# Optimization experiments

Hardware: AMD Instinct MI355X
Metric: run time of the kernel (lower is better)

The kernel has to match this reference:

```python
import jax, jax.numpy as jnp
import numpy as np

KSIZE = 13
PAD = KSIZE // 2
EPS = 1e-5
MIN_DISP = 1e-3  # clamp to avoid inf depth at zero disparity


def _unfold(x):
    # B,C,H,W -> B, C*k*k, H, W  (im2col with 'same' padding, stride 1; matches F.unfold)
    return jax.lax.conv_general_dilated_patches(
        x, filter_shape=(KSIZE, KSIZE), window_strides=(1, 1),
        padding=[(PAD, PAD), (PAD, PAD)])


def _znorm(p):
    # zero-mean, unit-norm over patch dim -> ZNCC becomes a plain dot product
    p = p - p.mean(axis=1, keepdims=True)
    return p / (jnp.linalg.norm(p, axis=1, keepdims=True) + EPS)


def setup_inputs() -> dict:
    key = jax.random.key(0)
    k1, k2 = jax.random.split(key)
    B, C, H, W = 1, 3, 192, 320
    l_image = jax.random.uniform(k1, (B, C, H, W), jnp.float32)
    # right image = horizontally shifted left + small noise so true matches exist
    r_image = jnp.roll(l_image, shift=-8, axis=-1) + 0.01 * jax.random.normal(k2, (B, C, H, W), jnp.float32)
    fx = 240.0
    intri = jnp.array([[[fx, 0.0, W / 2.0], [0.0, fx, H / 2.0], [0.0, 0.0, 1.0]]], jnp.float32)
    l_extri = jnp.eye(4, dtype=jnp.float32)[None]
    r_extri = l_extri.at[:, 0, 3].set(0.54)  # 0.54 m stereo baseline
    return {"l_image": l_image, "r_image": r_image, "l_intri": intri,
            "r_intri": intri, "l_extri": l_extri, "r_extri": r_extri}


def reference(l_image, r_image, l_intri, r_intri, l_extri, r_extri):
    B, C, H, W = l_image.shape
    # patch unfold (im2col) + ZNCC normalization
    ln = _znorm(_unfold(l_image).reshape(1, -1, H, W))  # 1,D,H,W
    rn = _znorm(_unfold(r_image).reshape(1, -1, H, W))
    # full-width correlation volume: each left pixel vs every right column in its row
    vol = jnp.einsum('bdhw,bdhv->bhwv', ln, rn)  # 1,H,W,W
    # reduce=True -> best-matching right column index
    corresp = jnp.argmax(vol, axis=-1).astype(l_image.dtype)  # 1,H,W
    disp = jnp.abs(corresp - jnp.arange(W, dtype=l_image.dtype))
    # disparity -> depth: depth = fx * baseline / disp
    fx = l_intri[:, 0, 0]
    rel = r_extri @ jnp.linalg.inv(l_extri)  # relative right<-left transform
    baseline = jnp.linalg.norm(rel[:, :3, 3], axis=-1)
    depth = fx[:, None, None] * baseline[:, None, None] / jnp.clip(disp, MIN_DISP, None)
    return depth
```

## Files before the change

### kernel.cpp

```cpp
#include <hip/hip_runtime.h>
#include <math.h>

#define HH 192
#define WW 320
#define DTOT 507.0f
#define KD 39
#define NSPAN 5
#define NCHUNK 5
#define XS 64
#define TV 64
#define TX 76
#define TU 80
#define TUW 76
#define TIS 76
#define TD2 77
#define NPIX (HH*WW)

__global__ void prep_kernel(const float* __restrict__ li, const float* __restrict__ le,
                            const float* __restrict__ re, float* __restrict__ sc,
                            unsigned long long* __restrict__ keys) {
    int t = blockIdx.x * blockDim.x + threadIdx.x;
    if (keys != nullptr && t < NPIX) keys[t] = 0ull;
    if (t == 0) {
        float a[4][4], inv[4][4];
        for (int i = 0; i < 4; ++i)
            for (int j = 0; j < 4; ++j) { a[i][j] = le[i*4+j]; inv[i][j] = (i == j) ? 1.0f : 0.0f; }
        for (int c = 0; c < 4; ++c) {
            int p = c; float mx = fabsf(a[c][c]);
            for (int r = c+1; r < 4; ++r) { float v = fabsf(a[r][c]); if (v > mx) { mx = v; p = r; } }
            if (p != c) for (int j = 0; j < 4; ++j) {
                float tq = a[c][j]; a[c][j] = a[p][j]; a[p][j] = tq;
                tq = inv[c][j]; inv[c][j] = inv[p][j]; inv[p][j] = tq;
            }
            float id = 1.0f / a[c][c];
            for (int j = 0; j < 4; ++j) { a[c][j] *= id; inv[c][j] *= id; }
            for (int r = 0; r < 4; ++r) if (r != c) {
                float f = a[r][c];
                for (int j = 0; j < 4; ++j) { a[r][j] -= f*a[c][j]; inv[r][j] -= f*inv[c][j]; }
            }
        }
        float rel[3];
        for (int i = 0; i < 3; ++i)
            rel[i] = re[i*4+0]*inv[0][3] + re[i*4+1]*inv[1][3] + re[i*4+2]*inv[2][3] + re[i*4+3]*inv[3][3];
        float baseline = sqrtf(rel[0]*rel[0] + rel[1]*rel[1] + rel[2]*rel[2]);
        sc[0] = li[0] * baseline;
    }
}

__global__ __launch_bounds__(256) void match_kernel(
        const float* __restrict__ limg, const float* __restrict__ rimg,
        unsigned long long* __restrict__ sink, int mode) {
    __shared__ float Ls[KD][TX];
    __shared__ float Rs[KD][TU];
    __shared__ float Tc[TU][TIS];
    __shared__ float colL[TX];
    __shared__ float colR1[TUW];
    __shared__ float colR2[TUW];
    __shared__ float smuR[TV];
    __shared__ float sivR[TV];
    __shared__ float redS[4][XS];
    __shared__ int   redV[4][XS];

    const int span = blockIdx.x;
    const int h    = blockIdx.y;
    const int ch   = blockIdx.z;
    const int wlo  = span * XS;
    const int ulo  = ch * TV;
    const int tid  = threadIdx.x;
    const int lane = tid & 63;
    const int wave = tid >> 6;

    for (int i2 = tid; i2 < KD*38; i2 += 256) {
        int k = i2 / 38, q = i2 - k*38;
        int c = k / 13, dy = k - c*13;
        int y = h - 6 + dy, x0 = wlo - 6 + 2*q;
        float2 v = make_float2(0.0f, 0.0f);
        if ((unsigned)y < (unsigned)HH) {
            const float* row = &limg[(c*HH + y)*WW];
            if ((unsigned)x0 < (unsigned)(WW-1)) {
                v = *(const float2*)&row[x0];
            } else {
                if ((unsigned)x0 < (unsigned)WW) v.x = row[x0];
                if ((unsigned)(x0+1) < (unsigned)WW) v.y = row[x0+1];
            }
        }
        *(float2*)&Ls[k][2*q] = v;
    }
    for (int i2 = tid; i2 < KD*40; i2 += 256) {
        int k = i2 / 40, q = i2 - k*40;
        int c = k / 13, dy = k - c*13;
        int y = h - 6 + dy, u0 = ulo - 6 + 2*q;
        float2 v = make_float2(0.0f, 0.0f);
        if ((unsigned)y < (unsigned)HH) {
            const float* row = &rimg[(c*HH + y)*WW];
            if ((unsigned)u0 < (unsigned)(WW-1)) {
                v = *(const float2*)&row[u0];
            } else {
                if ((unsigned)u0 < (unsigned)WW) v.x = row[u0];
                if ((unsigned)(u0+1) < (unsigned)WW) v.y = row[u0+1];
            }
        }
        *(float2*)&Rs[k][2*q] = v;
    }
    __syncthreads();

    if (tid < TX) {
        float s = 0.0f;
        for (int k = 0; k < KD; ++k) s += Ls[k][tid];
        colL[tid] = s;
    } else if (tid >= 128 && tid < 128 + TUW) {
        int c = tid - 128;
        float s1 = 0.0f, s2 = 0.0f;
        for (int k = 0; k < KD; ++k) {
            float v = Rs[k][c];
            s1 += v;
            s2 = fmaf(v, v, s2);
        }
        colR1[c] = s1;
        colR2[c] = s2;
    }
    __syncthreads();

    float muL;
    {
        float s = 0.0f;
        #pragma unroll
        for (int dx = 0; dx < 13; ++dx) s += colL[lane + dx];
        muL = s / DTOT;
    }

    if (tid < 190) {
        const int ti = tid % 19, tj = tid / 19;
        const int i0 = ti * 4, j0 = tj * 8;
        float a[4][8];
        #pragma unroll
        for (int r = 0; r < 4; ++r)
            #pragma unroll
            for (int c = 0; c < 8; ++c) a[r][c] = 0.0f;
        __builtin_amdgcn_s_setprio(1);
        for (int k = 0; k < KD; ++k) {
            float4 la = *(const float4*)&Ls[k][i0];
            float4 r0 = *(const float4*)&Rs[k][j0];
            float4 r1 = *(const float4*)&Rs[k][j0+4];
            float lx[4] = {la.x, la.y, la.z, la.w};
            float rx[8] = {r0.x, r0.y, r0.z, r0.w, r1.x, r1.y, r1.z, r1.w};
            #pragma unroll
            for (int r = 0; r < 4; ++r)
                #pragma unroll
                for (int c = 0; c < 8; ++c)
                    a[r][c] = fmaf(lx[r], rx[c], a[r][c]);
        }
        __builtin_amdgcn_s_setprio(0);
        #pragma unroll
        for (int c = 0; c < 8; ++c)
            *(float4*)&Tc[j0+c][i0] = make_float4(a[0][c], a[1][c], a[2][c], a[3][c]);
    } else if (tid >= 192) {
        int vcc = tid - 192;
        float s1 = 0.0f, s2 = 0.0f;
        #pragma unroll
        for (int dx = 0; dx < 13; ++dx) { s1 += colR1[vcc + dx]; s2 += colR2[vcc + dx]; }
        float mu = s1 / DTOT;
        float var = fmaxf(s2 - s1*s1/DTOT, 0.0f);
        smuR[vcc] = mu;
        sivR[vcc] = 1.0f / (sqrtf(var) + 1e-5f);
    }
    __syncthreads();

    float best = -1e30f;
    int bestv = 0;
    const float dml = DTOT * muL;
    for (int vi = 0; vi < 16; ++vi) {
        int vc = wave * 16 + vi;
        const float* tp0 = &Tc[vc][0] + lane;
        float S = 0.0f;
        int boff = 0;
        #pragma unroll
        for (int g = 0; g < 3; ++g) {
            asm volatile("" : "+v"(boff));
            float y0 = tp0[boff];
            float y1 = tp0[boff + TD2];
            float y2 = tp0[boff + 2*TD2];
            float y3 = tp0[boff + 3*TD2];
            S += y0; S += y1; S += y2; S += y3;
            boff += 4*TD2;
        }
        S += tp0[12*TD2];
        float score = (S - dml * smuR[vc]) * sivR[vc];
        int v = ulo + vc;
        if (score > best) { best = score; bestv = v; }
    }

    redS[wave][lane] = best;
    redV[wave][lane] = bestv;
    __syncthreads();
    if (tid < XS) {
        float b = redS[0][tid]; int bv = redV[0][tid];
        for (int wv = 1; wv < 4; ++wv) {
            float s = redS[wv][tid]; int v2 = redV[wv][tid];
            if (s > b || (s == b && v2 < bv)) { b = s; bv = v2; }
        }
        unsigned ob = __float_as_uint(b);
        ob = (ob & 0x80000000u) ? ~ob : (ob | 0x80000000u);
        unsigned long long key = ((unsigned long long)ob << 32) | (unsigned)(~(unsigned)bv);
        if (mode) {
            sink[(size_t)ch * NPIX + h*WW + wlo + tid] = key;
        } else {
            atomicMax(&sink[h*WW + wlo + tid], key);
        }
    }
}

__global__ __launch_bounds__(256) void depth_kernel(const unsigned long long* __restrict__ sink,
                                                    const float* __restrict__ sc,
                                                    float* __restrict__ out, int mode) {
    int t = blockIdx.x * 256 + threadIdx.x;
    unsigned long long k = sink[t];
    if (mode) {
        #pragma unroll
        for (int p = 1; p < NCHUNK; ++p) {
            unsigned long long k2 = sink[(size_t)p * NPIX + t];
            if (k2 > k) k = k2;
        }
    }
    int v = (int)(~(unsigned int)k);
    float w = (float)(t % WW);
    float disp = fmaxf(fabsf((float)v - w), 0.001f);
    out[t] = sc[0] / disp;
}

__global__ __launch_bounds__(256) void match_fallback(
        const float* __restrict__ limg, const float* __restrict__ rimg,
        const float* __restrict__ ws, float* __restrict__ out) {
    __shared__ float Ls[KD][76];
    __shared__ float Rs[KD][76];
    __shared__ float Tt[76][81];
    __shared__ float colL[76];
    __shared__ float colR1[76];
    __shared__ float colR2[76];
    __shared__ float smuR[64];
    __shared__ float sivR[64];
    __shared__ float redS[4][64];
    __shared__ int   redV[4][64];

    const int span = blockIdx.x;
    const int h    = blockIdx.y;
    const int wlo  = span * 64;
    const int tid  = threadIdx.x;
    const int lane = tid & 63;
    const int wave = tid >> 6;

    for (int i = tid; i < KD*76; i += 256) {
        int k = i / 76, xl = i % 76;
        int c = k / 13, dy = k % 13;
        int y = h - 6 + dy, x = wlo - 6 + xl;
        float v = 0.0f;
        if (y >= 0 && y < HH && x >= 0 && x < WW) v = limg[(c*HH + y)*WW + x];
        Ls[k][xl] = v;
    }
    __syncthreads();

    if (tid < 76) {
        float s = 0.0f;
        for (int k = 0; k < KD; ++k) s += Ls[k][tid];
        colL[tid] = s;
    }
    __syncthreads();

    float muL;
    {
        float s = 0.0f;
        #pragma unroll
        for (int dx = 0; dx < 13; ++dx) s += colL[lane + dx];
        muL = s / DTOT;
    }

    float best = -1e30f;
    int bestv = 0;

    for (int ch = 0; ch < NCHUNK; ++ch) {
        const int ulo = ch * 64;
        for (int i = tid; i < KD*76; i += 256) {
            int k = i / 76, uc = i % 76;
            int c = k / 13, dy = k % 13;
            int y = h - 6 + dy, u = ulo - 6 + uc;
            float v = 0.0f;
            if (y >= 0 && y < HH && u >= 0 && u < WW) v = rimg[(c*HH + y)*WW + u];
            Rs[k][uc] = v;
        }
        __syncthreads();

        if (tid < 76) {
            float s1 = 0.0f, s2 = 0.0f;
            for (int k = 0; k < KD; ++k) {
                float v = Rs[k][tid];
                s1 += v;
                s2 = fmaf(v, v, s2);
            }
            colR1[tid] = s1;
            colR2[tid] = s2;
        }

        for (int t = tid; t < 361; t += 256) {
            int ti = t % 19, tj = t / 19;
            int i0 = ti * 4, j0 = tj * 4;
            float a00=0,a01=0,a02=0,a03=0, a10=0,a11=0,a12=0,a13=0;
            float a20=0,a21=0,a22=0,a23=0, a30=0,a31=0,a32=0,a33=0;
            for (int k = 0; k < KD; ++k) {
                float4 la = *(const float4*)&Ls[k][i0];
                float4 rb = *(const float4*)&Rs[k][j0];
                a00 = fmaf(la.x, rb.x, a00); a01 = fmaf(la.x, rb.y, a01);
                a02 = fmaf(la.x, rb.z, a02); a03 = fmaf(la.x, rb.w, a03);
                a10 = fmaf(la.y, rb.x, a10); a11 = fmaf(la.y, rb.y, a11);
                a12 = fmaf(la.y, rb.z, a12); a13 = fmaf(la.y, rb.w, a13);
                a20 = fmaf(la.z, rb.x, a20); a21 = fmaf(la.z, rb.y, a21);
                a22 = fmaf(la.z, rb.z, a22); a23 = fmaf(la.z, rb.w, a23);
                a30 = fmaf(la.w, rb.x, a30); a31 = fmaf(la.w, rb.y, a31);
                a32 = fmaf(la.w, rb.z, a32); a33 = fmaf(la.w, rb.w, a33);
            }
            float* tr0 = &Tt[i0+0][j0]; tr0[0]=a00; tr0[1]=a01; tr0[2]=a02; tr0[3]=a03;
            float* tr1 = &Tt[i0+1][j0]; tr1[0]=a10; tr1[1]=a11; tr1[2]=a12; tr1[3]=a13;
            float* tr2 = &Tt[i0+2][j0]; tr2[0]=a20; tr2[1]=a21; tr2[2]=a22; tr2[3]=a23;
            float* tr3 = &Tt[i0+3][j0]; tr3[0]=a30; tr3[1]=a31; tr3[2]=a32; tr3[3]=a33;
        }
        __syncthreads();

        if (tid < 64) {
            float s1 = 0.0f, s2 = 0.0f;
            #pragma unroll
            for (int dx = 0; dx < 13; ++dx) { s1 += colR1[tid + dx]; s2 += colR2[tid + dx]; }
            float mu = s1 / DTOT;
            float var = fmaxf(s2 - s1*s1/DTOT, 0.0f);
            smuR[tid] = mu;
            sivR[tid] = 1.0f / (sqrtf(var) + 1e-5f);
        }
        __syncthreads();

        for (int vi = 0; vi < 16; ++vi) {
            int vc = wave * 16 + vi;
            int v  = ulo + vc;
            const float* tp = &Tt[lane][vc];
            float S = 0.0f;
            #pragma unroll
            for (int dxp = 0; dxp < 13; ++dxp)
                S += tp[dxp * 82];
            float score = (S - DTOT * muL * smuR[vc]) * sivR[vc];
            if (score > best) { best = score; bestv = v; }
        }
    }

    redS[wave][lane] = best;
    redV[wave][lane] = bestv;
    __syncthreads();
    if (tid < 64) {
        float b = redS[0][tid]; int bv = redV[0][tid];
        for (int wv = 1; wv < 4; ++wv) {
            float s = redS[wv][tid]; int v2 = redV[wv][tid];
            if (s > b || (s == b && v2 < bv)) { b = s; bv = v2; }
        }
        int w = wlo + tid;
        float disp = fabsf((float)bv - (float)w);
        disp = fmaxf(disp, 0.001f);
        out[h*WW + w] = ws[0] / disp;
    }
}

extern "C" void kernel_launch(void* const* d_in, const int* in_sizes, int n_in,
                              void* d_out, int out_size, void* d_ws, size_t ws_size,
                              hipStream_t stream) {
    const float* limg   = (const float*)d_in[0];
    const float* rimg   = (const float*)d_in[1];
    const float* lintri = (const float*)d_in[2];
    const float* lex    = (const float*)d_in[4];
    const float* rex    = (const float*)d_in[5];
    float* out = (float*)d_out;
    float* scp = (float*)d_ws;

    const size_t needA = 8 + (size_t)NCHUNK * NPIX * 8;
    const size_t needB = 8 + (size_t)NPIX * 8;
    if (ws_size >= needA) {
        unsigned long long* planes = (unsigned long long*)d_ws + 1;
        hipLaunchKernelGGL(prep_kernel, dim3(1), dim3(64), 0, stream,
                           lintri, lex, rex, scp, (unsigned long long*)nullptr);
        hipLaunchKernelGGL(match_kernel, dim3(NSPAN, HH, NCHUNK), dim3(256), 0, stream,
                           limg, rimg, planes, 1);
        hipLaunchKernelGGL(depth_kernel, dim3(NPIX/256), dim3(256), 0, stream,
                           planes, scp, out, 1);
    } else if (ws_size >= needB) {
        unsigned long long* keys = (unsigned long long*)d_ws + 1;
        hipLaunchKernelGGL(prep_kernel, dim3(NPIX/256), dim3(256), 0, stream,
                           lintri, lex, rex, scp, keys);
        hipLaunchKernelGGL(match_kernel, dim3(NSPAN, HH, NCHUNK), dim3(256), 0, stream,
                           limg, rimg, keys, 0);
        hipLaunchKernelGGL(depth_kernel, dim3(NPIX/256), dim3(256), 0, stream,
                           keys, scp, out, 0);
    } else {
        hipLaunchKernelGGL(prep_kernel, dim3(1), dim3(64), 0, stream,
                           lintri, lex, rex, scp, (unsigned long long*)nullptr);
        hipLaunchKernelGGL(match_fallback, dim3(NSPAN, HH), dim3(256), 0, stream,
                           limg, rimg, scp, out);
    }
}
```

Baseline: 142.3 us.

## Merge column-sum stage into GEMM phase and use packed FMA accumulators

Removes a separate block-wide barrier stage by having wave 3 (idle during the tile product) compute the left/right column sums and right-patch mean and inverse std while waves 0-2 do the correlation tile. The inner product accumulators are rewritten as 2-wide vectors so the compiler can emit packed FP32 FMA instructions. This drops one __syncthreads and overlaps the stats work with the matmul, but puts all stats on one wave, which could lengthen the critical path if that wave finishes after the others.

```diff
diff --git a/kernel.cpp b/kernel.cpp
--- a/kernel.cpp
+++ b/kernel.cpp
@@ -15,6 +15,8 @@
 #define TIS 76
 #define TD2 77
 #define NPIX (HH*WW)
+
+typedef float v2f __attribute__((ext_vector_type(2)));
 
 __global__ void prep_kernel(const float* __restrict__ li, const float* __restrict__ le,
                             const float* __restrict__ re, float* __restrict__ sc,
@@ -104,71 +106,78 @@
     }
     __syncthreads();
 
-    if (tid < TX) {
-        float s = 0.0f;
-        for (int k = 0; k < KD; ++k) s += Ls[k][tid];
-        colL[tid] = s;
-    } else if (tid >= 128 && tid < 128 + TUW) {
-        int c = tid - 128;
-        float s1 = 0.0f, s2 = 0.0f;
-        for (int k = 0; k < KD; ++k) {
-            float v = Rs[k][c];
-            s1 += v;
-            s2 = fmaf(v, v, s2);
-        }
-        colR1[c] = s1;
-        colR2[c] = s2;
-    }
-    __syncthreads();
-
-    float muL;
-    {
-        float s = 0.0f;
-        #pragma unroll
-        for (int dx = 0; dx < 13; ++dx) s += colL[lane + dx];
-        muL = s / DTOT;
-    }
-
     if (tid < 190) {
         const int ti = tid % 19, tj = tid / 19;
         const int i0 = ti * 4, j0 = tj * 8;
-        float a[4][8];
+        v2f acc[4][4];
         #pragma unroll
         for (int r = 0; r < 4; ++r)
             #pragma unroll
-            for (int c = 0; c < 8; ++c) a[r][c] = 0.0f;
+            for (int c2 = 0; c2 < 4; ++c2) acc[r][c2] = (v2f){0.0f, 0.0f};
         __builtin_amdgcn_s_setprio(1);
         for (int k = 0; k < KD; ++k) {
             float4 la = *(const float4*)&Ls[k][i0];
             float4 r0 = *(const float4*)&Rs[k][j0];
             float4 r1 = *(const float4*)&Rs[k][j0+4];
+            v2f rp0 = {r0.x, r0.y}, rp1 = {r0.z, r0.w};
+            v2f rp2 = {r1.x, r1.y}, rp3 = {r1.z, r1.w};
             float lx[4] = {la.x, la.y, la.z, la.w};
-            float rx[8] = {r0.x, r0.y, r0.z, r0.w, r1.x, r1.y, r1.z, r1.w};
             #pragma unroll
-            for (int r = 0; r < 4; ++r)
-                #pragma unroll
-                for (int c = 0; c < 8; ++c)
-                    a[r][c] = fmaf(lx[r], rx[c], a[r][c]);
+            for (int r = 0; r < 4; ++r) {
+                v2f lb = {lx[r], lx[r]};
+                acc[r][0] = __builtin_elementwise_fma(lb, rp0, acc[r][0]);
+                acc[r][1] = __builtin_elementwise_fma(lb, rp1, acc[r][1]);
+                acc[r][2] = __builtin_elementwise_fma(lb, rp2, acc[r][2]);
+                acc[r][3] = __builtin_elementwise_fma(lb, rp3, acc[r][3]);
+            }
         }
         __builtin_amdgcn_s_setprio(0);
         #pragma unroll
-        for (int c = 0; c < 8; ++c)
-            *(float4*)&Tc[j0+c][i0] = make_float4(a[0][c], a[1][c], a[2][c], a[3][c]);
-    } else if (tid >= 192) {
-        int vcc = tid - 192;
-        float s1 = 0.0f, s2 = 0.0f;
-        #pragma unroll
-        for (int dx = 0; dx < 13; ++dx) { s1 += colR1[vcc + dx]; s2 += colR2[vcc + dx]; }
-        float mu = s1 / DTOT;
-        float var = fmaxf(s2 - s1*s1/DTOT, 0.0f);
-        smuR[vcc] = mu;
-        sivR[vcc] = 1.0f / (sqrtf(var) + 1e-5f);
-    }
-    __syncthreads();
+        for (int c = 0; c < 8; ++c) {
+            float4 wv = make_float4(acc[0][c>>1][c&1], acc[1][c>>1][c&1],
+                                    acc[2][c>>1][c&1], acc[3][c>>1][c&1]);
+            *(float4*)&Tc[j0+c][i0] = wv;
+        }
+    } else if (wave == 3) {
+        for (int c = lane; c < TX; c += 64) {
+            float s = 0.0f;
+            for (int k = 0; k < KD; ++k) s += Ls[k][c];
+            colL[c] = s;
+        }
+        for (int c = lane; c < TUW; c += 64) {
+            float s1 = 0.0f, s2 = 0.0f;
+            for (int k = 0; k < KD; ++k) {
+                float v = Rs[k][c];
+                s1 += v;
+                s2 = fmaf(v, v, s2);
+            }
+            colR1[c] = s1;
+            colR2[c] = s2;
+        }
+        asm volatile("s_waitcnt lgkmcnt(0)" ::: "memory");
+        {
+            float s1 = 0.0f, s2 = 0.0f;
+            #pragma unroll
+            for (int dx = 0; dx < 13; ++dx) { s1 += colR1[lane + dx]; s2 += colR2[lane + dx]; }
+            float mu = s1 / DTOT;
+            float var = fmaxf(s2 - s1*s1/DTOT, 0.0f);
+            smuR[lane] = mu;
+            sivR[lane] = 1.0f / (sqrtf(var) + 1e-5f);
+        }
+    }
+    __syncthreads();
+
+    float muL;
+    {
+        float s = 0.0f;
+        #pragma unroll
+        for (int dx = 0; dx < 13; ++dx) s += colL[lane + dx];
+        muL = s / DTOT;
+    }
+    const float dml = DTOT * muL;
 
     float best = -1e30f;
     int bestv = 0;
-    const float dml = DTOT * muL;
     for (int vi = 0; vi < 16; ++vi) {
         int vc = wave * 16 + vi;
         const float* tp0 = &Tc[vc][0] + lane;
```

After: 137.0 us. -3.7%, faster.
